# Kernel tuning notes

Hardware: AMD Instinct MI355X
Metric: run time of the kernel (lower is better)

## Reference

```python
import jax, jax.numpy as jnp
import numpy as np

NUM_BINS = 256


def setup_inputs() -> dict:
    key = jax.random.key(0)
    x = jax.random.uniform(key, (64, 3, 512, 512), dtype=jnp.float32)
    return {"x": x}


def _otsu_thresholds(hist):
    # hist: [B, 256] float counts. Returns per-image Otsu threshold [B] (int).
    bins = jnp.arange(NUM_BINS, dtype=jnp.float32)
    p = hist / jnp.sum(hist, axis=-1, keepdims=True)
    omega = jnp.cumsum(p, axis=-1)                 # class-0 weight up to t
    mu = jnp.cumsum(bins * p, axis=-1)             # class-0 first moment
    mu_t = mu[:, -1:]                              # total mean
    denom = omega * (1.0 - omega)
    # between-class variance; invalid where one class is empty
    sigma_b = jnp.where(denom > 1e-12,
                        (mu_t * omega - mu) ** 2 / jnp.maximum(denom, 1e-12),
                        -1.0)
    return jnp.argmax(sigma_b, axis=-1)            # [B]


def reference(x):
    # Emulate (x*255).astype(uint8): truncation toward zero, clipped to [0,255]
    u8 = jnp.clip(jnp.floor(x * 255.0), 0.0, 255.0)          # [B,3,H,W]
    # cv2 RGB->GRAY: round(0.299 R + 0.587 G + 0.114 B)
    gray = jnp.clip(jnp.round(0.299 * u8[:, 0] + 0.587 * u8[:, 1] + 0.114 * u8[:, 2]),
                    0.0, 255.0).astype(jnp.int32)            # [B,H,W]
    B = gray.shape[0]
    flat = gray.reshape(B, -1)
    # per-image 256-bin histogram via batched scatter-add
    hist = jnp.zeros((B, NUM_BINS), jnp.float32).at[
        jnp.arange(B)[:, None], flat].add(1.0)
    t = _otsu_thresholds(hist)                               # [B]
    # cv2 THRESH_BINARY: pixel > thresh -> 255; module divides by 255 -> {0,1}
    mask = (gray > t[:, None, None]).astype(jnp.int64)       # [B,H,W]
    return mask
```

## Files before the change

kernel.cpp:

```cpp
#include <hip/hip_runtime.h>

#define NUM_BINS 256
#define HW 262144
#define NBATCH 64

__device__ __forceinline__ int gray_px(float r, float g, float b) {
#pragma clang fp contract(off)
    float ur = fminf(fmaxf(floorf(r * 255.0f), 0.0f), 255.0f);
    float ug = fminf(fmaxf(floorf(g * 255.0f), 0.0f), 255.0f);
    float ub = fminf(fmaxf(floorf(b * 255.0f), 0.0f), 255.0f);
    float s = 0.299f * ur + 0.587f * ug + 0.114f * ub;
    s = fminf(fmaxf(rintf(s), 0.0f), 255.0f);
    return (int)s;
}

__global__ void init_hist_k(unsigned int* __restrict__ hist) {
    hist[(blockIdx.x << 8) + threadIdx.x] = 0u;
}

__global__ void __launch_bounds__(256)
gray_hist_k(const float* __restrict__ x, unsigned char* __restrict__ gray,
            unsigned int* __restrict__ hist) {
    __shared__ unsigned int lh[NUM_BINS];
    const int t = threadIdx.x;
    lh[t] = 0u;
    __syncthreads();

    const int b     = blockIdx.x >> 6;
    const int chunk = blockIdx.x & 63;
    const size_t base = (size_t)b * 3 * HW;
    const float4* xr = (const float4*)(x + base);
    const float4* xg = (const float4*)(x + base + HW);
    const float4* xb = (const float4*)(x + base + 2 * HW);
    uchar4* gout = gray ? (uchar4*)(gray + (size_t)b * HW) : nullptr;

#pragma unroll
    for (int i = 0; i < 4; ++i) {
        const int vidx = (chunk << 10) + (i << 8) + t;
        float4 r4 = xr[vidx];
        float4 g4 = xg[vidx];
        float4 b4 = xb[vidx];
        int g0 = gray_px(r4.x, g4.x, b4.x);
        int g1 = gray_px(r4.y, g4.y, b4.y);
        int g2 = gray_px(r4.z, g4.z, b4.z);
        int g3 = gray_px(r4.w, g4.w, b4.w);
        if (gout) gout[vidx] = make_uchar4((unsigned char)g0, (unsigned char)g1,
                                           (unsigned char)g2, (unsigned char)g3);
        atomicAdd(&lh[g0], 1u);
        atomicAdd(&lh[g1], 1u);
        atomicAdd(&lh[g2], 1u);
        atomicAdd(&lh[g3], 1u);
    }
    __syncthreads();
    atomicAdd(&hist[(b << 8) + t], lh[t]);
}

__global__ void __launch_bounds__(64)
otsu_k(const unsigned int* __restrict__ hist, int* __restrict__ thr) {
    const int b = threadIdx.x;
    const unsigned int* h = hist + (b << 8);
    const float invN = 1.0f / 262144.0f;

    float mu_t = 0.0f;
    for (int i = 0; i < NUM_BINS; ++i) {
#pragma clang fp contract(off)
        float p = (float)h[i] * invN;
        mu_t += (float)i * p;
    }

    float omega = 0.0f, mu = 0.0f;
    float best = -3.0f;
    int bi = 0;
    for (int i = 0; i < NUM_BINS; ++i) {
#pragma clang fp contract(off)
        float p = (float)h[i] * invN;
        omega += p;
        mu += (float)i * p;
        float denom = omega * (1.0f - omega);
        float s;
        if (denom > 1e-12f) {
            float d = mu_t * omega - mu;
            s = (d * d) / fmaxf(denom, 1e-12f);
        } else {
            s = -1.0f;
        }
        if (s > best) { best = s; bi = i; }
    }
    thr[b] = bi;
}

__global__ void __launch_bounds__(256)
mask_gray_k(const unsigned char* __restrict__ gray, const int* __restrict__ thr,
            int* __restrict__ out) {
    const int b     = blockIdx.x >> 8;
    const int chunk = blockIdx.x & 255;
    const int vidx  = (chunk << 8) + threadIdx.x;
    const int th = thr[b];
    uchar4 g = ((const uchar4*)(gray + (size_t)b * HW))[vidx];
    int4 o;
    o.x = ((int)g.x > th) ? 1 : 0;
    o.y = ((int)g.y > th) ? 1 : 0;
    o.z = ((int)g.z > th) ? 1 : 0;
    o.w = ((int)g.w > th) ? 1 : 0;
    ((int4*)(out + (size_t)b * HW))[vidx] = o;
}

__global__ void __launch_bounds__(256)
mask_x_k(const float* __restrict__ x, const int* __restrict__ thr,
         int* __restrict__ out) {
    const int b     = blockIdx.x >> 8;
    const int chunk = blockIdx.x & 255;
    const int vidx  = (chunk << 8) + threadIdx.x;
    const int th = thr[b];
    const size_t base = (size_t)b * 3 * HW;
    float4 r4 = ((const float4*)(x + base))[vidx];
    float4 g4 = ((const float4*)(x + base + HW))[vidx];
    float4 b4 = ((const float4*)(x + base + 2 * HW))[vidx];
    int4 o;
    o.x = (gray_px(r4.x, g4.x, b4.x) > th) ? 1 : 0;
    o.y = (gray_px(r4.y, g4.y, b4.y) > th) ? 1 : 0;
    o.z = (gray_px(r4.z, g4.z, b4.z) > th) ? 1 : 0;
    o.w = (gray_px(r4.w, g4.w, b4.w) > th) ? 1 : 0;
    ((int4*)(out + (size_t)b * HW))[vidx] = o;
}

extern "C" void kernel_launch(void* const* d_in, const int* in_sizes, int n_in,
                              void* d_out, int out_size, void* d_ws, size_t ws_size,
                              hipStream_t stream) {
    const float* x = (const float*)d_in[0];
    int* out = (int*)d_out;
    unsigned char* ws = (unsigned char*)d_ws;

    const size_t grayBytes = (size_t)NBATCH * HW;
    const size_t histBytes = (size_t)NBATCH * NUM_BINS * 4;
    const bool useGray = ws_size >= grayBytes + histBytes + 256;

    unsigned char* gray = useGray ? ws : nullptr;
    unsigned int* hist = (unsigned int*)(ws + (useGray ? grayBytes : 0));
    int* thr = (int*)((unsigned char*)hist + histBytes);

    init_hist_k<<<NBATCH, NUM_BINS, 0, stream>>>(hist);
    gray_hist_k<<<NBATCH * 64, 256, 0, stream>>>(x, gray, hist);
    otsu_k<<<1, 64, 0, stream>>>(hist, thr);
    if (useGray)
        mask_gray_k<<<NBATCH * 256, 256, 0, stream>>>(gray, thr, out);
    else
        mask_x_k<<<NBATCH * 256, 256, 0, stream>>>(x, thr, out);
}
```

Measured before the change: 344.7 us.

## Fuse gray, histogram, Otsu and mask into one cooperative kernel with grid sync

Replaces the four-kernel pipeline with a single cooperative kernel that keeps packed gray values in registers across a grid-wide sync. Each block writes a partial histogram, then after the sync sums its image's partials, computes the Otsu threshold, and writes the mask directly. This removes the gray-image round trip through global memory and the extra launches. In exchange it needs all 1024 blocks co-resident, adds a grid barrier, and runs a serial single-thread Otsu scan in every block. It falls back to the old path if the cooperative launch fails; that fallback now assumes the workspace is large enough.

```diff
diff --git a/kernel.cpp b/kernel.cpp
--- a/kernel.cpp
+++ b/kernel.cpp
@@ -1,8 +1,14 @@
 #include <hip/hip_runtime.h>
+#include <hip/hip_cooperative_groups.h>
+
+namespace cg = cooperative_groups;
 
 #define NUM_BINS 256
 #define HW 262144
 #define NBATCH 64
+#define BPB 16
+#define GRID (NBATCH * BPB)
+#define ITERS 16
 
 __device__ __forceinline__ int gray_px(float r, float g, float b) {
 #pragma clang fp contract(off)
@@ -14,6 +20,103 @@
     return (int)s;
 }
 
+__device__ __forceinline__ int otsu_from_hist(const unsigned int* h) {
+    const float invN = 1.0f / 262144.0f;
+    float mu_t = 0.0f;
+    for (int i = 0; i < NUM_BINS; ++i) {
+#pragma clang fp contract(off)
+        float p = (float)h[i] * invN;
+        mu_t += (float)i * p;
+    }
+    float omega = 0.0f, mu = 0.0f, best = -3.0f;
+    int bi = 0;
+    for (int i = 0; i < NUM_BINS; ++i) {
+#pragma clang fp contract(off)
+        float p = (float)h[i] * invN;
+        omega += p;
+        mu += (float)i * p;
+        float denom = omega * (1.0f - omega);
+        float sig;
+        if (denom > 1e-12f) {
+            float d = mu_t * omega - mu;
+            sig = (d * d) / fmaxf(denom, 1e-12f);
+        } else {
+            sig = -1.0f;
+        }
+        if (sig > best) { best = sig; bi = i; }
+    }
+    return bi;
+}
+
+__global__ void __launch_bounds__(256, 4)
+fused_otsu_k(const float* __restrict__ x, int* __restrict__ out,
+             unsigned int* __restrict__ partial) {
+    __shared__ unsigned int lh[4][NUM_BINS];
+    __shared__ unsigned int bh[NUM_BINS];
+    __shared__ int th_s;
+    const int t = threadIdx.x;
+    const int wv = t >> 6;
+
+#pragma unroll
+    for (int w = 0; w < 4; ++w) lh[w][t] = 0u;
+    __syncthreads();
+
+    const int b   = blockIdx.x >> 4;
+    const int sub = blockIdx.x & 15;
+    const size_t base = (size_t)b * 3 * HW;
+    const float4* xr = (const float4*)(x + base);
+    const float4* xg = (const float4*)(x + base + HW);
+    const float4* xb = (const float4*)(x + base + 2 * HW);
+
+    unsigned int gpack[ITERS];
+#pragma unroll
+    for (int k = 0; k < ITERS; ++k) {
+        const int vidx = (sub << 12) + (k << 8) + t;
+        float4 r4 = xr[vidx];
+        float4 g4 = xg[vidx];
+        float4 b4 = xb[vidx];
+        int g0 = gray_px(r4.x, g4.x, b4.x);
+        int g1 = gray_px(r4.y, g4.y, b4.y);
+        int g2 = gray_px(r4.z, g4.z, b4.z);
+        int g3 = gray_px(r4.w, g4.w, b4.w);
+        gpack[k] = (unsigned)g0 | ((unsigned)g1 << 8) |
+                   ((unsigned)g2 << 16) | ((unsigned)g3 << 24);
+        atomicAdd(&lh[wv][g0], 1u);
+        atomicAdd(&lh[wv][g1], 1u);
+        atomicAdd(&lh[wv][g2], 1u);
+        atomicAdd(&lh[wv][g3], 1u);
+    }
+    __syncthreads();
+    partial[((size_t)blockIdx.x << 8) + t] =
+        lh[0][t] + lh[1][t] + lh[2][t] + lh[3][t];
+
+    cg::this_grid().sync();
+
+    unsigned int s = 0;
+    const unsigned int* pb = partial + (((size_t)b * BPB) << 8);
+#pragma unroll
+    for (int c = 0; c < BPB; ++c) s += pb[(c << 8) + t];
+    bh[t] = s;
+    __syncthreads();
+
+    if (t == 0) th_s = otsu_from_hist(bh);
+    __syncthreads();
+    const int th = th_s;
+
+    int4* ob = (int4*)(out + (size_t)b * HW);
+#pragma unroll
+    for (int k = 0; k < ITERS; ++k) {
+        const int vidx = (sub << 12) + (k << 8) + t;
+        const unsigned g = gpack[k];
+        int4 o;
+        o.x = ((int)(g & 255u)         > th) ? 1 : 0;
+        o.y = ((int)((g >> 8) & 255u)  > th) ? 1 : 0;
+        o.z = ((int)((g >> 16) & 255u) > th) ? 1 : 0;
+        o.w = ((int)(g >> 24)          > th) ? 1 : 0;
+        ob[vidx] = o;
+    }
+}
+
 __global__ void init_hist_k(unsigned int* __restrict__ hist) {
     hist[(blockIdx.x << 8) + threadIdx.x] = 0u;
 }
@@ -25,15 +128,13 @@
     const int t = threadIdx.x;
     lh[t] = 0u;
     __syncthreads();
-
     const int b     = blockIdx.x >> 6;
     const int chunk = blockIdx.x & 63;
     const size_t base = (size_t)b * 3 * HW;
     const float4* xr = (const float4*)(x + base);
     const float4* xg = (const float4*)(x + base + HW);
     const float4* xb = (const float4*)(x + base + 2 * HW);
-    uchar4* gout = gray ? (uchar4*)(gray + (size_t)b * HW) : nullptr;
-
+    uchar4* gout = (uchar4*)(gray + (size_t)b * HW);
 #pragma unroll
     for (int i = 0; i < 4; ++i) {
         const int vidx = (chunk << 10) + (i << 8) + t;
@@ -44,8 +145,8 @@
         int g1 = gray_px(r4.y, g4.y, b4.y);
         int g2 = gray_px(r4.z, g4.z, b4.z);
         int g3 = gray_px(r4.w, g4.w, b4.w);
-        if (gout) gout[vidx] = make_uchar4((unsigned char)g0, (unsigned char)g1,
-                                           (unsigned char)g2, (unsigned char)g3);
+        gout[vidx] = make_uchar4((unsigned char)g0, (unsigned char)g1,
+                                 (unsigned char)g2, (unsigned char)g3);
         atomicAdd(&lh[g0], 1u);
         atomicAdd(&lh[g1], 1u);
         atomicAdd(&lh[g2], 1u);
@@ -58,35 +159,9 @@
 __global__ void __launch_bounds__(64)
 otsu_k(const unsigned int* __restrict__ hist, int* __restrict__ thr) {
     const int b = threadIdx.x;
-    const unsigned int* h = hist + (b << 8);
-    const float invN = 1.0f / 262144.0f;
-
-    float mu_t = 0.0f;
-    for (int i = 0; i < NUM_BINS; ++i) {
-#pragma clang fp contract(off)
-        float p = (float)h[i] * invN;
-        mu_t += (float)i * p;
-    }
-
-    float omega = 0.0f, mu = 0.0f;
-    float best = -3.0f;
-    int bi = 0;
-    for (int i = 0; i < NUM_BINS; ++i) {
-#pragma clang fp contract(off)
-        float p = (float)h[i] * invN;
-        omega += p;
-        mu += (float)i * p;
-        float denom = omega * (1.0f - omega);
-        float s;
-        if (denom > 1e-12f) {
-            float d = mu_t * omega - mu;
-            s = (d * d) / fmaxf(denom, 1e-12f);
-        } else {
-            s = -1.0f;
-        }
-        if (s > best) { best = s; bi = i; }
-    }
-    thr[b] = bi;
+    unsigned int h[1];
+    (void)h;
+    thr[b] = otsu_from_hist(hist + (b << 8));
 }
 
 __global__ void __launch_bounds__(256)
@@ -105,25 +180,6 @@
     ((int4*)(out + (size_t)b * HW))[vidx] = o;
 }
 
-__global__ void __launch_bounds__(256)
-mask_x_k(const float* __restrict__ x, const int* __restrict__ thr,
-         int* __restrict__ out) {
-    const int b     = blockIdx.x >> 8;
-    const int chunk = blockIdx.x & 255;
-    const int vidx  = (chunk << 8) + threadIdx.x;
-    const int th = thr[b];
-    const size_t base = (size_t)b * 3 * HW;
-    float4 r4 = ((const float4*)(x + base))[vidx];
-    float4 g4 = ((const float4*)(x + base + HW))[vidx];
-    float4 b4 = ((const float4*)(x + base + 2 * HW))[vidx];
-    int4 o;
-    o.x = (gray_px(r4.x, g4.x, b4.x) > th) ? 1 : 0;
-    o.y = (gray_px(r4.y, g4.y, b4.y) > th) ? 1 : 0;
-    o.z = (gray_px(r4.z, g4.z, b4.z) > th) ? 1 : 0;
-    o.w = (gray_px(r4.w, g4.w, b4.w) > th) ? 1 : 0;
-    ((int4*)(out + (size_t)b * HW))[vidx] = o;
-}
-
 extern "C" void kernel_launch(void* const* d_in, const int* in_sizes, int n_in,
                               void* d_out, int out_size, void* d_ws, size_t ws_size,
                               hipStream_t stream) {
@@ -131,19 +187,19 @@
     int* out = (int*)d_out;
     unsigned char* ws = (unsigned char*)d_ws;
 
-    const size_t grayBytes = (size_t)NBATCH * HW;
-    const size_t histBytes = (size_t)NBATCH * NUM_BINS * 4;
-    const bool useGray = ws_size >= grayBytes + histBytes + 256;
-
-    unsigned char* gray = useGray ? ws : nullptr;
-    unsigned int* hist = (unsigned int*)(ws + (useGray ? grayBytes : 0));
-    int* thr = (int*)((unsigned char*)hist + histBytes);
-
-    init_hist_k<<<NBATCH, NUM_BINS, 0, stream>>>(hist);
-    gray_hist_k<<<NBATCH * 64, 256, 0, stream>>>(x, gray, hist);
-    otsu_k<<<1, 64, 0, stream>>>(hist, thr);
-    if (useGray)
+    unsigned int* partial = (unsigned int*)ws;
+    unsigned int* hist = (unsigned int*)(ws + (1u << 20));
+    int* thr = (int*)(ws + (1u << 20) + NBATCH * NUM_BINS * 4);
+
+    void* args[] = { (void*)&x, (void*)&out, (void*)&partial };
+    hipError_t err = hipLaunchCooperativeKernel((const void*)fused_otsu_k,
+                                                dim3(GRID), dim3(256),
+                                                args, 0, stream);
+    if (err != hipSuccess) {
+        unsigned char* gray = ws + (2u << 20);
+        init_hist_k<<<NBATCH, NUM_BINS, 0, stream>>>(hist);
+        gray_hist_k<<<NBATCH * 64, 256, 0, stream>>>(x, gray, hist);
+        otsu_k<<<1, 64, 0, stream>>>(hist, thr);
         mask_gray_k<<<NBATCH * 256, 256, 0, stream>>>(gray, thr, out);
-    else
-        mask_x_k<<<NBATCH * 256, 256, 0, stream>>>(x, thr, out);
-}
+    }
+}
```

Result: slower. 445.8 us (+29.3%).
